# Performance work log

Measured on AMD Instinct MI355X. Metric: run time of the kernel, lower is better.

Reference implementation:

```python
import jax, jax.numpy as jnp
import numpy as np

N_SAMPLES = 64000
SAMPLE_RATE = 16000
DEPTH = 64              # bins per sinusoid in frequencies_softmax
HZ_MIN, HZ_MAX = 20.0, 8000.0


def exp_sigmoid(x, exponent=10.0, max_value=2.0, threshold=1e-7):
    # ddsp.core.exp_sigmoid
    return max_value * jax.nn.sigmoid(x) ** jnp.log(exponent) + threshold


def unit_to_hz(unit):
    # log-scale (midi) mapping of [0,1] -> [HZ_MIN, HZ_MAX]
    midi_min = 69.0 + 12.0 * np.log2(HZ_MIN / 440.0)
    midi_max = 69.0 + 12.0 * np.log2(HZ_MAX / 440.0)
    midi = midi_min + unit * (midi_max - midi_min)
    return 440.0 * 2.0 ** ((midi - 69.0) / 12.0)


def frequencies_softmax(logits):
    # ddsp.core.frequencies_softmax: softmax attention over DEPTH unit bins per sinusoid
    b, t, nd = logits.shape
    logits = logits.reshape(b, t, nd // DEPTH, DEPTH)
    probs = jax.nn.softmax(logits, axis=-1)
    bins = jnp.linspace(0.0, 1.0, DEPTH).astype(logits.dtype)
    f_unit = jnp.sum(probs * bins, axis=-1)          # [B, T, N]
    return unit_to_hz(f_unit)


def upsample_with_windows(x, n_timesteps):
    # ddsp.core.upsample_with_windows (add_endpoint=True): hann-window overlap-add at
    b, t, c = x.shape
    hop = n_timesteps // t
    xp = jnp.concatenate([x, x[:, -1:, :]], axis=1)  # pad endpoint frame -> [B, T+1, C]
    s = jnp.arange(n_timesteps)
    k = s // hop
    r = (s % hop).astype(x.dtype)
    w = 0.5 - 0.5 * jnp.cos(jnp.pi * r / hop)        # weight of next frame
    x0 = jnp.take(xp, k, axis=1)
    x1 = jnp.take(xp, k + 1, axis=1)
    return x0 * (1.0 - w)[None, :, None] + x1 * w[None, :, None]


def resample_linear(x, n_timesteps):
    # ddsp.core.resample(method='linear', add_endpoint=True): scale = T / n_timesteps
    b, t, c = x.shape
    src = jnp.arange(n_timesteps).astype(x.dtype) * (t / n_timesteps)
    i0 = jnp.clip(jnp.floor(src).astype(jnp.int32), 0, t - 1)
    i1 = jnp.clip(i0 + 1, 0, t - 1)
    frac = (src - i0.astype(x.dtype))[None, :, None]
    return jnp.take(x, i0, axis=1) * (1.0 - frac) + jnp.take(x, i1, axis=1) * frac


def setup_inputs() -> dict:
    key = jax.random.key(0)
    k1, k2 = jax.random.split(key)
    amplitudes = jax.random.normal(k1, (4, 250, 100), dtype=jnp.float32)
    frequencies = jax.random.normal(k2, (4, 250, 6400), dtype=jnp.float32)
    return {"amplitudes": amplitudes, "frequencies": frequencies}


def reference(amplitudes, frequencies):
    # get_controls
    amps = exp_sigmoid(amplitudes)                                   # [B, T, N]
    freqs = frequencies_softmax(frequencies)                         # [B, T, N] in Hz
    amps = amps * (freqs < SAMPLE_RATE / 2.0).astype(amps.dtype)     # remove_above_nyquist
    # get_signal
    amp_env = upsample_with_windows(amps, N_SAMPLES)                 # [B, S, N]
    freq_env = resample_linear(freqs, N_SAMPLES)                     # [B, S, N]
    omegas = freq_env * (2.0 * jnp.pi / SAMPLE_RATE)                 # rad/sample
    phases = jnp.cumsum(omegas, axis=1)                              # cumulative phase scan
    return jnp.sum(amp_env * jnp.sin(phases), axis=-1)               # [B, S]
```

## Files before the change

kernel.cpp:

```cpp
#include <hip/hip_runtime.h>
#include <math.h>


#define Bb 4
#define Tt 250
#define Nn 100
#define HOP 256
#define NSMP 64000

#define LOG2_400F 8.6438561897747247f

__global__ __launch_bounds__(256) void ctrl_kernel(
    const float* __restrict__ amp_in,
    const float* __restrict__ logits,
    float* __restrict__ fq,
    float* __restrict__ amp_out,
    int n_sids)
{
    const int wave = threadIdx.x >> 6;
    const int lane = threadIdx.x & 63;
    const int grp  = lane >> 4;
    const int sub  = lane & 15;
    const int sid  = blockIdx.x * 16 + wave * 4 + grp;
    if (sid >= n_sids) return;

    const float4 x4 = *(const float4*)(logits + (size_t)sid * 64 + sub * 4);

    const float e0 = __expf(x4.x);
    const float e1 = __expf(x4.y);
    const float e2 = __expf(x4.z);
    const float e3 = __expf(x4.w);
    const float bb = (float)(sub * 4);
    float den = (e0 + e1) + (e2 + e3);
    float num = e0 * bb + e1 * (bb + 1.0f) + e2 * (bb + 2.0f) + e3 * (bb + 3.0f);

#pragma unroll
    for (int off = 1; off < 16; off <<= 1) {
        num += __shfl_xor(num, off, 64);
        den += __shfl_xor(den, off, 64);
    }

    if (sub == 0) {
        const float u = num / (den * 63.0f);
        const float f = 20.0f * exp2f(u * LOG2_400F);
        fq[sid] = f;
        const float xa = amp_in[sid];
        const float sg = 1.0f / (1.0f + __expf(-xa));
        float av = 2.0f * __expf(2.3025851f * __logf(sg)) + 1e-7f;
        av = (f < 8000.0f) ? av : 0.0f;
        amp_out[sid] = av;
    }
}

__global__ __launch_bounds__(256) void scan_kernel(
    const float* __restrict__ fq,
    float* __restrict__ Pf)
{
    __shared__ double wtot[4];
    const int b = blockIdx.x / Nn;
    const int n = blockIdx.x % Nn;
    const int k = threadIdx.x;
    const int wave = k >> 6;
    const int lane = k & 63;

    double S = 0.0;
    if (k < Tt) {
        const int kp = (k + 1 < Tt) ? (k + 1) : (Tt - 1);
        const double f0 = (double)fq[(size_t)(b * Tt + k) * Nn + n];
        const double f1 = (double)fq[(size_t)(b * Tt + kp) * Nn + n];
        S = (256.0 * f0 + 127.5 * (f1 - f0)) * (1.0 / 16000.0);
    }

    double inc = S;
#pragma unroll
    for (int off = 1; off < 64; off <<= 1) {
        const double v = __shfl_up(inc, off, 64);
        if (lane >= off) inc += v;
    }
    if (lane == 63) wtot[wave] = inc;
    __syncthreads();

    double base = 0.0;
#pragma unroll
    for (int w = 0; w < 3; ++w)
        if (w < wave) base += wtot[w];

    if (k < Tt) {
        const double P = base + inc - S;
        Pf[(size_t)(b * Tt + k) * Nn + n] = (float)(P - floor(P));
    }
}

__global__ __launch_bounds__(256) void synth_kernel(
    const float* __restrict__ fq,
    const float* __restrict__ amp,
    const float* __restrict__ Pf,
    float* __restrict__ out)
{
    __shared__ float4 c4[2][Nn];
    __shared__ float  pfs[2][Nn];
    const int pair = blockIdx.x % (Tt / 2);
    const int b    = blockIdx.x / (Tt / 2);
    const int k0   = pair * 2;
    const int tid  = threadIdx.x;

    if (tid < 2 * Nn) {
        const int h = tid / Nn;
        const int n = tid % Nn;
        const int k = k0 + h;
        const int kp = (k + 1 < Tt) ? (k + 1) : (Tt - 1);
        const size_t i0 = (size_t)(b * Tt + k) * Nn + n;
        const size_t i1 = (size_t)(b * Tt + kp) * Nn + n;
        const float a0 = amp[i0];
        const float a1 = amp[i1];
        const float f0 = fq[i0];
        const float f1 = fq[i1];
        float4 c;
        c.x = a0;
        c.y = a1 - a0;
        c.z = f0 * (1.0f / 16000.0f);
        c.w = (f1 - f0) * (1.0f / (16000.0f * 256.0f));
        c4[h][n] = c;
        pfs[h][n] = Pf[i0];
    }
    __syncthreads();

    const int h  = tid >> 7;
    const int r0 = tid & 127;
    const int k  = k0 + h;
    const int rB = r0 + 128;

    const float wA = 0.5f - 0.5f * __builtin_amdgcn_cosf((float)r0 * (1.0f / 512.0f));
    const float wB = 0.5f - 0.5f * __builtin_amdgcn_cosf((float)rB * (1.0f / 512.0f));
    const float rp1A = (float)(r0 + 1);
    const float rp1B = (float)(rB + 1);
    const float triA = (float)(r0 * (r0 + 1) / 2);
    const float triB = (float)(rB * (rB + 1) / 2);

    float sumA = 0.0f, sumB = 0.0f;
#pragma unroll 4
    for (int n = 0; n < Nn; ++n) {
        const float4 c = c4[h][n];
        const float pf = pfs[h][n];
        const float aA = c.x + c.y * wA;
        const float aB = c.x + c.y * wB;
        float phA = pf + rp1A * c.z + triA * c.w;
        float phB = pf + rp1B * c.z + triB * c.w;
        phA -= floorf(phA);
        phB -= floorf(phB);
        sumA += aA * __builtin_amdgcn_sinf(phA);
        sumB += aB * __builtin_amdgcn_sinf(phB);
    }
    float* o = out + (size_t)b * NSMP + (size_t)k * HOP;
    o[r0] = sumA;
    o[rB] = sumB;
}

extern "C" void kernel_launch(void* const* d_in, const int* in_sizes, int n_in,
                              void* d_out, int out_size, void* d_ws, size_t ws_size,
                              hipStream_t stream) {
    const float* amps_in = (const float*)d_in[0];
    const float* logits  = (const float*)d_in[1];
    float* out = (float*)d_out;

    const int n_sids = in_sizes[0];
    char* ws = (char*)d_ws;
    float* fqw  = (float*)ws;
    float* ampw = (float*)(ws + 400000);
    float* Pf   = (float*)(ws + 800000);

    const int ctrl_blocks = (n_sids + 15) / 16;
    ctrl_kernel<<<dim3(ctrl_blocks), dim3(256), 0, stream>>>(amps_in, logits, fqw, ampw, n_sids);
    scan_kernel<<<dim3(Bb * Nn), dim3(256), 0, stream>>>(fqw, Pf);
    synth_kernel<<<dim3(Bb * (Tt / 2)), dim3(256), 0, stream>>>(fqw, ampw, Pf, out);
}
```

Measured before the change: 86.75 us.

## Fuse phase scan into synth kernel via per-block redundant prefix sums

Removes the separate scan kernel and its workspace round-trip. Each synth block now computes the prefix sum of frequencies up to its frame by serially summing the column in double precision, split between two halves of the block. This saves a kernel launch and a global write and read, but adds redundant O(T) loads per block, up to about 250 strided reads per thread for late frames, which creates load imbalance.

```diff
diff --git a/kernel.cpp b/kernel.cpp
--- a/kernel.cpp
+++ b/kernel.cpp
@@ -52,57 +52,33 @@
     }
 }
 
-__global__ __launch_bounds__(256) void scan_kernel(
-    const float* __restrict__ fq,
-    float* __restrict__ Pf)
-{
-    __shared__ double wtot[4];
-    const int b = blockIdx.x / Nn;
-    const int n = blockIdx.x % Nn;
-    const int k = threadIdx.x;
-    const int wave = k >> 6;
-    const int lane = k & 63;
-
-    double S = 0.0;
-    if (k < Tt) {
-        const int kp = (k + 1 < Tt) ? (k + 1) : (Tt - 1);
-        const double f0 = (double)fq[(size_t)(b * Tt + k) * Nn + n];
-        const double f1 = (double)fq[(size_t)(b * Tt + kp) * Nn + n];
-        S = (256.0 * f0 + 127.5 * (f1 - f0)) * (1.0 / 16000.0);
-    }
-
-    double inc = S;
-#pragma unroll
-    for (int off = 1; off < 64; off <<= 1) {
-        const double v = __shfl_up(inc, off, 64);
-        if (lane >= off) inc += v;
-    }
-    if (lane == 63) wtot[wave] = inc;
-    __syncthreads();
-
-    double base = 0.0;
-#pragma unroll
-    for (int w = 0; w < 3; ++w)
-        if (w < wave) base += wtot[w];
-
-    if (k < Tt) {
-        const double P = base + inc - S;
-        Pf[(size_t)(b * Tt + k) * Nn + n] = (float)(P - floor(P));
-    }
-}
-
 __global__ __launch_bounds__(256) void synth_kernel(
     const float* __restrict__ fq,
     const float* __restrict__ amp,
-    const float* __restrict__ Pf,
     float* __restrict__ out)
 {
     __shared__ float4 c4[2][Nn];
     __shared__ float  pfs[2][Nn];
+    __shared__ double halfsum[2][Nn];
+
     const int pair = blockIdx.x % (Tt / 2);
     const int b    = blockIdx.x / (Tt / 2);
     const int k0   = pair * 2;
     const int tid  = threadIdx.x;
+
+    {
+        const int half = tid >> 7;
+        const int nc   = tid & 127;
+        if (nc < Nn) {
+            const float* col = fq + (size_t)b * Tt * Nn + nc;
+            double s = 0.0;
+#pragma unroll 4
+            for (int j = 1 + half; j < k0; j += 2)
+                s += (double)col[(size_t)j * Nn];
+            halfsum[half][nc] = s;
+        }
+    }
+    __syncthreads();
 
     if (tid < 2 * Nn) {
         const int h = tid / Nn;
@@ -121,7 +97,19 @@
         c.z = f0 * (1.0f / 16000.0f);
         c.w = (f1 - f0) * (1.0f / (16000.0f * 256.0f));
         c4[h][n] = c;
-        pfs[h][n] = Pf[i0];
+
+        float pf = 0.0f;
+        if (k > 0) {
+            double sum = halfsum[0][n] + halfsum[1][n];
+            if (h == 1 && k0 >= 1)
+                sum += (double)fq[(size_t)(b * Tt + k0) * Nn + n];
+            const double fz = (double)fq[(size_t)(b * Tt) * Nn + n];
+            double P = (128.5 * fz + 256.0 * sum + 127.5 * (double)f0)
+                       * (1.0 / 16000.0);
+            P -= floor(P);
+            pf = (float)P;
+        }
+        pfs[h][n] = pf;
     }
     __syncthreads();
 
@@ -167,10 +155,8 @@
     char* ws = (char*)d_ws;
     float* fqw  = (float*)ws;
     float* ampw = (float*)(ws + 400000);
-    float* Pf   = (float*)(ws + 800000);
 
     const int ctrl_blocks = (n_sids + 15) / 16;
     ctrl_kernel<<<dim3(ctrl_blocks), dim3(256), 0, stream>>>(amps_in, logits, fqw, ampw, n_sids);
-    scan_kernel<<<dim3(Bb * Nn), dim3(256), 0, stream>>>(fqw, Pf);
-    synth_kernel<<<dim3(Bb * (Tt / 2)), dim3(256), 0, stream>>>(fqw, ampw, Pf, out);
+    synth_kernel<<<dim3(Bb * (Tt / 2)), dim3(256), 0, stream>>>(fqw, ampw, out);
 }
```

Result: slower. 91.64 us (+5.6%).

## Fuse three kernels into one cooperative kernel with grid-wide syncs

Applied to the files above, without the earlier changes.

Merges the control, scan and synthesis kernels into one cooperative launch of 500 blocks, separated by two grid-wide barriers. The control stage becomes a grid-stride loop and the scan runs on the first 400 blocks. This is meant to remove two kernel launch gaps and their inter-kernel drain. In exchange it pays the cost of two grid syncs, and the cooperative launch needs every block resident at once, which the launch_bounds hint of two blocks per CU supports.

```diff
diff --git a/kernel.cpp b/kernel.cpp
--- a/kernel.cpp
+++ b/kernel.cpp
@@ -1,5 +1,8 @@
 #include <hip/hip_runtime.h>
+#include <hip/hip_cooperative_groups.h>
 #include <math.h>
+
+namespace cg = cooperative_groups;
 
 
 #define Bb 4
@@ -7,153 +10,154 @@
 #define Nn 100
 #define HOP 256
 #define NSMP 64000
+#define GRID_BLOCKS (Bb * (Tt / 2))
 
 #define LOG2_400F 8.6438561897747247f
 
-__global__ __launch_bounds__(256) void ctrl_kernel(
+__global__ __launch_bounds__(256, 2) void fused_kernel(
     const float* __restrict__ amp_in,
     const float* __restrict__ logits,
     float* __restrict__ fq,
-    float* __restrict__ amp_out,
+    float* __restrict__ amp,
+    float* __restrict__ Pf,
+    float* __restrict__ out,
     int n_sids)
 {
-    const int wave = threadIdx.x >> 6;
-    const int lane = threadIdx.x & 63;
-    const int grp  = lane >> 4;
-    const int sub  = lane & 15;
-    const int sid  = blockIdx.x * 16 + wave * 4 + grp;
-    if (sid >= n_sids) return;
+    __shared__ double wtot[4];
+    __shared__ float4 c4[2][Nn];
+    __shared__ float  pfs[2][Nn];
 
-    const float4 x4 = *(const float4*)(logits + (size_t)sid * 64 + sub * 4);
+    const int tid  = threadIdx.x;
+    const int wave = tid >> 6;
+    const int lane = tid & 63;
 
-    const float e0 = __expf(x4.x);
-    const float e1 = __expf(x4.y);
-    const float e2 = __expf(x4.z);
-    const float e3 = __expf(x4.w);
-    const float bb = (float)(sub * 4);
-    float den = (e0 + e1) + (e2 + e3);
-    float num = e0 * bb + e1 * (bb + 1.0f) + e2 * (bb + 2.0f) + e3 * (bb + 3.0f);
+    {
+        const int grp = lane >> 4;
+        const int sub = lane & 15;
+        for (int base = blockIdx.x * 16; base < n_sids; base += GRID_BLOCKS * 16) {
+            const int sid = base + wave * 4 + grp;
+            const float4 x4 = *(const float4*)(logits + (size_t)sid * 64 + sub * 4);
+
+            const float e0 = __expf(x4.x);
+            const float e1 = __expf(x4.y);
+            const float e2 = __expf(x4.z);
+            const float e3 = __expf(x4.w);
+            const float bb = (float)(sub * 4);
+            float den = (e0 + e1) + (e2 + e3);
+            float num = e0 * bb + e1 * (bb + 1.0f) + e2 * (bb + 2.0f) + e3 * (bb + 3.0f);
 
 #pragma unroll
-    for (int off = 1; off < 16; off <<= 1) {
-        num += __shfl_xor(num, off, 64);
-        den += __shfl_xor(den, off, 64);
+            for (int off = 1; off < 16; off <<= 1) {
+                num += __shfl_xor(num, off, 64);
+                den += __shfl_xor(den, off, 64);
+            }
+
+            if (sub == 0) {
+                const float u = num / (den * 63.0f);
+                const float f = 20.0f * exp2f(u * LOG2_400F);
+                fq[sid] = f;
+                const float xa = amp_in[sid];
+                const float sg = 1.0f / (1.0f + __expf(-xa));
+                float av = 2.0f * __expf(2.3025851f * __logf(sg)) + 1e-7f;
+                av = (f < 8000.0f) ? av : 0.0f;
+                amp[sid] = av;
+            }
+        }
     }
 
-    if (sub == 0) {
-        const float u = num / (den * 63.0f);
-        const float f = 20.0f * exp2f(u * LOG2_400F);
-        fq[sid] = f;
-        const float xa = amp_in[sid];
-        const float sg = 1.0f / (1.0f + __expf(-xa));
-        float av = 2.0f * __expf(2.3025851f * __logf(sg)) + 1e-7f;
-        av = (f < 8000.0f) ? av : 0.0f;
-        amp_out[sid] = av;
-    }
-}
+    cg::this_grid().sync();
 
-__global__ __launch_bounds__(256) void scan_kernel(
-    const float* __restrict__ fq,
-    float* __restrict__ Pf)
-{
-    __shared__ double wtot[4];
-    const int b = blockIdx.x / Nn;
-    const int n = blockIdx.x % Nn;
-    const int k = threadIdx.x;
-    const int wave = k >> 6;
-    const int lane = k & 63;
+    if (blockIdx.x < Bb * Nn) {
+        const int b = blockIdx.x / Nn;
+        const int n = blockIdx.x % Nn;
+        const int k = tid;
 
-    double S = 0.0;
-    if (k < Tt) {
-        const int kp = (k + 1 < Tt) ? (k + 1) : (Tt - 1);
-        const double f0 = (double)fq[(size_t)(b * Tt + k) * Nn + n];
-        const double f1 = (double)fq[(size_t)(b * Tt + kp) * Nn + n];
-        S = (256.0 * f0 + 127.5 * (f1 - f0)) * (1.0 / 16000.0);
+        double S = 0.0;
+        if (k < Tt) {
+            const int kp = (k + 1 < Tt) ? (k + 1) : (Tt - 1);
+            const double f0 = (double)fq[(size_t)(b * Tt + k) * Nn + n];
+            const double f1 = (double)fq[(size_t)(b * Tt + kp) * Nn + n];
+            S = (256.0 * f0 + 127.5 * (f1 - f0)) * (1.0 / 16000.0);
+        }
+
+        double inc = S;
+#pragma unroll
+        for (int off = 1; off < 64; off <<= 1) {
+            const double v = __shfl_up(inc, off, 64);
+            if (lane >= off) inc += v;
+        }
+        if (lane == 63) wtot[wave] = inc;
+        __syncthreads();
+
+        double base = 0.0;
+#pragma unroll
+        for (int w = 0; w < 3; ++w)
+            if (w < wave) base += wtot[w];
+
+        if (k < Tt) {
+            const double P = base + inc - S;
+            Pf[(size_t)(b * Tt + k) * Nn + n] = (float)(P - floor(P));
+        }
     }
 
-    double inc = S;
-#pragma unroll
-    for (int off = 1; off < 64; off <<= 1) {
-        const double v = __shfl_up(inc, off, 64);
-        if (lane >= off) inc += v;
+    cg::this_grid().sync();
+
+    {
+        const int pair = blockIdx.x % (Tt / 2);
+        const int b    = blockIdx.x / (Tt / 2);
+        const int k0   = pair * 2;
+
+        if (tid < 2 * Nn) {
+            const int h = tid / Nn;
+            const int n = tid % Nn;
+            const int k = k0 + h;
+            const int kp = (k + 1 < Tt) ? (k + 1) : (Tt - 1);
+            const size_t i0 = (size_t)(b * Tt + k) * Nn + n;
+            const size_t i1 = (size_t)(b * Tt + kp) * Nn + n;
+            const float a0 = amp[i0];
+            const float a1 = amp[i1];
+            const float f0 = fq[i0];
+            const float f1 = fq[i1];
+            float4 c;
+            c.x = a0;
+            c.y = a1 - a0;
+            c.z = f0 * (1.0f / 16000.0f);
+            c.w = (f1 - f0) * (1.0f / (16000.0f * 256.0f));
+            c4[h][n] = c;
+            pfs[h][n] = Pf[i0];
+        }
+        __syncthreads();
+
+        const int h  = tid >> 7;
+        const int r0 = tid & 127;
+        const int k  = k0 + h;
+        const int rB = r0 + 128;
+
+        const float wA = 0.5f - 0.5f * __builtin_amdgcn_cosf((float)r0 * (1.0f / 512.0f));
+        const float wB = 0.5f - 0.5f * __builtin_amdgcn_cosf((float)rB * (1.0f / 512.0f));
+        const float rp1A = (float)(r0 + 1);
+        const float rp1B = (float)(rB + 1);
+        const float triA = (float)(r0 * (r0 + 1) / 2);
+        const float triB = (float)(rB * (rB + 1) / 2);
+
+        float sumA = 0.0f, sumB = 0.0f;
+#pragma unroll 4
+        for (int n = 0; n < Nn; ++n) {
+            const float4 c = c4[h][n];
+            const float pf = pfs[h][n];
+            const float aA = c.x + c.y * wA;
+            const float aB = c.x + c.y * wB;
+            float phA = pf + rp1A * c.z + triA * c.w;
+            float phB = pf + rp1B * c.z + triB * c.w;
+            phA -= floorf(phA);
+            phB -= floorf(phB);
+            sumA += aA * __builtin_amdgcn_sinf(phA);
+            sumB += aB * __builtin_amdgcn_sinf(phB);
+        }
+        float* o = out + (size_t)b * NSMP + (size_t)k * HOP;
+        o[r0] = sumA;
+        o[rB] = sumB;
     }
-    if (lane == 63) wtot[wave] = inc;
-    __syncthreads();
-
-    double base = 0.0;
-#pragma unroll
-    for (int w = 0; w < 3; ++w)
-        if (w < wave) base += wtot[w];
-
-    if (k < Tt) {
-        const double P = base + inc - S;
-        Pf[(size_t)(b * Tt + k) * Nn + n] = (float)(P - floor(P));
-    }
-}
-
-__global__ __launch_bounds__(256) void synth_kernel(
-    const float* __restrict__ fq,
-    const float* __restrict__ amp,
-    const float* __restrict__ Pf,
-    float* __restrict__ out)
-{
-    __shared__ float4 c4[2][Nn];
-    __shared__ float  pfs[2][Nn];
-    const int pair = blockIdx.x % (Tt / 2);
-    const int b    = blockIdx.x / (Tt / 2);
-    const int k0   = pair * 2;
-    const int tid  = threadIdx.x;
-
-    if (tid < 2 * Nn) {
-        const int h = tid / Nn;
-        const int n = tid % Nn;
-        const int k = k0 + h;
-        const int kp = (k + 1 < Tt) ? (k + 1) : (Tt - 1);
-        const size_t i0 = (size_t)(b * Tt + k) * Nn + n;
-        const size_t i1 = (size_t)(b * Tt + kp) * Nn + n;
-        const float a0 = amp[i0];
-        const float a1 = amp[i1];
-        const float f0 = fq[i0];
-        const float f1 = fq[i1];
-        float4 c;
-        c.x = a0;
-        c.y = a1 - a0;
-        c.z = f0 * (1.0f / 16000.0f);
-        c.w = (f1 - f0) * (1.0f / (16000.0f * 256.0f));
-        c4[h][n] = c;
-        pfs[h][n] = Pf[i0];
-    }
-    __syncthreads();
-
-    const int h  = tid >> 7;
-    const int r0 = tid & 127;
-    const int k  = k0 + h;
-    const int rB = r0 + 128;
-
-    const float wA = 0.5f - 0.5f * __builtin_amdgcn_cosf((float)r0 * (1.0f / 512.0f));
-    const float wB = 0.5f - 0.5f * __builtin_amdgcn_cosf((float)rB * (1.0f / 512.0f));
-    const float rp1A = (float)(r0 + 1);
-    const float rp1B = (float)(rB + 1);
-    const float triA = (float)(r0 * (r0 + 1) / 2);
-    const float triB = (float)(rB * (rB + 1) / 2);
-
-    float sumA = 0.0f, sumB = 0.0f;
-#pragma unroll 4
-    for (int n = 0; n < Nn; ++n) {
-        const float4 c = c4[h][n];
-        const float pf = pfs[h][n];
-        const float aA = c.x + c.y * wA;
-        const float aB = c.x + c.y * wB;
-        float phA = pf + rp1A * c.z + triA * c.w;
-        float phB = pf + rp1B * c.z + triB * c.w;
-        phA -= floorf(phA);
-        phB -= floorf(phB);
-        sumA += aA * __builtin_amdgcn_sinf(phA);
-        sumB += aB * __builtin_amdgcn_sinf(phB);
-    }
-    float* o = out + (size_t)b * NSMP + (size_t)k * HOP;
-    o[r0] = sumA;
-    o[rB] = sumB;
 }
 
 extern "C" void kernel_launch(void* const* d_in, const int* in_sizes, int n_in,
@@ -163,14 +167,16 @@
     const float* logits  = (const float*)d_in[1];
     float* out = (float*)d_out;
 
-    const int n_sids = in_sizes[0];
+    int n_sids = in_sizes[0];
     char* ws = (char*)d_ws;
     float* fqw  = (float*)ws;
     float* ampw = (float*)(ws + 400000);
-    float* Pf   = (float*)(ws + 800000);
+    float* Pfw  = (float*)(ws + 800000);
 
-    const int ctrl_blocks = (n_sids + 15) / 16;
-    ctrl_kernel<<<dim3(ctrl_blocks), dim3(256), 0, stream>>>(amps_in, logits, fqw, ampw, n_sids);
-    scan_kernel<<<dim3(Bb * Nn), dim3(256), 0, stream>>>(fqw, Pf);
-    synth_kernel<<<dim3(Bb * (Tt / 2)), dim3(256), 0, stream>>>(fqw, ampw, Pf, out);
+    void* args[] = {
+        (void*)&amps_in, (void*)&logits, (void*)&fqw, (void*)&ampw,
+        (void*)&Pfw, (void*)&out, (void*)&n_sids
+    };
+    hipLaunchCooperativeKernel((const void*)fused_kernel,
+                               dim3(GRID_BLOCKS), dim3(256), args, 0, stream);
 }
```

Result: slower. 203.7 us (+134.9%).

## Fuse softmax control computation into per-column phase scan kernel

Applied to the files above, without the earlier changes.

Merges the control kernel and the scan kernel into one. Each block now owns one (batch, sinusoid) column, and each thread computes the 64-bin softmax frequency and the amplitude for its frame serially. The frequencies are shared through LDS for the prefix scan instead of being re-read from global memory. This removes a kernel launch and a global round trip, but the logits reads become strided across threads (each lane reads its own 256-byte row) rather than coalesced, and each thread holds 64 extra registers for the loaded logits.

```diff
diff --git a/kernel.cpp b/kernel.cpp
--- a/kernel.cpp
+++ b/kernel.cpp
@@ -10,64 +10,58 @@
 
 #define LOG2_400F 8.6438561897747247f
 
-__global__ __launch_bounds__(256) void ctrl_kernel(
+__global__ __launch_bounds__(256) void ctrl_scan_kernel(
     const float* __restrict__ amp_in,
     const float* __restrict__ logits,
     float* __restrict__ fq,
-    float* __restrict__ amp_out,
-    int n_sids)
+    float* __restrict__ amp,
+    float* __restrict__ Pf)
 {
-    const int wave = threadIdx.x >> 6;
-    const int lane = threadIdx.x & 63;
-    const int grp  = lane >> 4;
-    const int sub  = lane & 15;
-    const int sid  = blockIdx.x * 16 + wave * 4 + grp;
-    if (sid >= n_sids) return;
+    __shared__ float  fcol[256];
+    __shared__ double wtot[4];
 
-    const float4 x4 = *(const float4*)(logits + (size_t)sid * 64 + sub * 4);
+    const int b    = blockIdx.x / Nn;
+    const int n    = blockIdx.x % Nn;
+    const int k    = threadIdx.x;
+    const int wave = k >> 6;
+    const int lane = k & 63;
 
-    const float e0 = __expf(x4.x);
-    const float e1 = __expf(x4.y);
-    const float e2 = __expf(x4.z);
-    const float e3 = __expf(x4.w);
-    const float bb = (float)(sub * 4);
-    float den = (e0 + e1) + (e2 + e3);
-    float num = e0 * bb + e1 * (bb + 1.0f) + e2 * (bb + 2.0f) + e3 * (bb + 3.0f);
+    float f = 0.0f;
+    if (k < Tt) {
+        const size_t sid = (size_t)(b * Tt + k) * Nn + n;
+        const float4* lp = (const float4*)(logits + sid * 64);
+        float4 v[16];
+#pragma unroll
+        for (int i = 0; i < 16; ++i) v[i] = lp[i];
+        const float xa = amp_in[sid];
 
+        float num = 0.0f, den = 0.0f;
 #pragma unroll
-    for (int off = 1; off < 16; off <<= 1) {
-        num += __shfl_xor(num, off, 64);
-        den += __shfl_xor(den, off, 64);
-    }
+        for (int i = 0; i < 16; ++i) {
+            const float bb = (float)(i * 4);
+            const float e0 = __expf(v[i].x);
+            const float e1 = __expf(v[i].y);
+            const float e2 = __expf(v[i].z);
+            const float e3 = __expf(v[i].w);
+            den += (e0 + e1) + (e2 + e3);
+            num += e0 * bb + e1 * (bb + 1.0f) + e2 * (bb + 2.0f) + e3 * (bb + 3.0f);
+        }
+        const float u = num / (den * 63.0f);
+        f = 20.0f * exp2f(u * LOG2_400F);
+        fq[sid] = f;
 
-    if (sub == 0) {
-        const float u = num / (den * 63.0f);
-        const float f = 20.0f * exp2f(u * LOG2_400F);
-        fq[sid] = f;
-        const float xa = amp_in[sid];
         const float sg = 1.0f / (1.0f + __expf(-xa));
         float av = 2.0f * __expf(2.3025851f * __logf(sg)) + 1e-7f;
         av = (f < 8000.0f) ? av : 0.0f;
-        amp_out[sid] = av;
+        amp[sid] = av;
     }
-}
-
-__global__ __launch_bounds__(256) void scan_kernel(
-    const float* __restrict__ fq,
-    float* __restrict__ Pf)
-{
-    __shared__ double wtot[4];
-    const int b = blockIdx.x / Nn;
-    const int n = blockIdx.x % Nn;
-    const int k = threadIdx.x;
-    const int wave = k >> 6;
-    const int lane = k & 63;
+    fcol[k] = f;
+    __syncthreads();
 
     double S = 0.0;
     if (k < Tt) {
-        const int kp = (k + 1 < Tt) ? (k + 1) : (Tt - 1);
-        const double f0 = (double)fq[(size_t)(b * Tt + k) * Nn + n];
-        const double f1 = (double)fq[(size_t)(b * Tt + kp) * Nn + n];
+        const double f0 = (double)f;
+        const double f1 = (double)((k + 1 < Tt) ? fcol[k + 1] : f);
         S = (256.0 * f0 + 127.5 * (f1 - f0)) * (1.0 / 16000.0);
     }
 
@@ -163,14 +157,11 @@
     const float* logits  = (const float*)d_in[1];
     float* out = (float*)d_out;
 
-    const int n_sids = in_sizes[0];
     char* ws = (char*)d_ws;
     float* fqw  = (float*)ws;
     float* ampw = (float*)(ws + 400000);
-    float* Pf   = (float*)(ws + 800000);
+    float* Pfw  = (float*)(ws + 800000);
 
-    const int ctrl_blocks = (n_sids + 15) / 16;
-    ctrl_kernel<<<dim3(ctrl_blocks), dim3(256), 0, stream>>>(amps_in, logits, fqw, ampw, n_sids);
-    scan_kernel<<<dim3(Bb * Nn), dim3(256), 0, stream>>>(fqw, Pf);
-    synth_kernel<<<dim3(Bb * (Tt / 2)), dim3(256), 0, stream>>>(fqw, ampw, Pf, out);
+    ctrl_scan_kernel<<<dim3(Bb * Nn), dim3(256), 0, stream>>>(amps_in, logits, fqw, ampw, Pfw);
+    synth_kernel<<<dim3(Bb * (Tt / 2)), dim3(256), 0, stream>>>(fqw, ampw, Pfw, out);
 }
```

Result: no change. 85.96 us (-0.9%).
